# Optimization experiments

Hardware: AMD Instinct MI355X
Metric: run time of the kernel (lower is better)

## Reference

```python
import jax, jax.numpy as jnp
import numpy as np

B, N_OBJS, HW = 2, 30, 64
W_H = HW * HW                      # 4096 visual tokens
N = W_H + 4 * N_OBJS + 64          # 4280 total tokens (satisfies the N - 4*n_objs - 64 == 64*64 check)
QUERY_DIM, HEADS, DIM_HEAD = 320, 8, 40
INNER = HEADS * DIM_HEAD


def setup_inputs() -> dict:
    key = jax.random.key(0)
    ks = jax.random.split(key, 7)
    x = jax.random.normal(ks[0], (B, N, QUERY_DIM), dtype=jnp.float32)
    # binary per-object instance masks on the 64x64 visual grid
    att_masks = (jax.random.uniform(ks[1], (B, N_OBJS, HW, HW)) < 0.15).astype(jnp.float32)
    s = 0.02
    Wq = jax.random.normal(ks[2], (QUERY_DIM, INNER), dtype=jnp.float32) * s
    Wk = jax.random.normal(ks[3], (QUERY_DIM, INNER), dtype=jnp.float32) * s
    Wv = jax.random.normal(ks[4], (QUERY_DIM, INNER), dtype=jnp.float32) * s
    Wo = jax.random.normal(ks[5], (INNER, QUERY_DIM), dtype=jnp.float32) * s
    bo = jax.random.normal(ks[6], (QUERY_DIM,), dtype=jnp.float32) * s
    return {"x": x, "att_masks": att_masks, "Wq": Wq, "Wk": Wk, "Wv": Wv, "Wo": Wo, "bo": bo}


def _build_mask(att_masks):
    # att_masks: [B, n_objs, 64, 64] -> additive/boolean grounding mask [B, 1, N, N]
    b, n_objs = att_masks.shape[0], att_masks.shape[1]
    m = att_masks.reshape(b, n_objs, W_H)                     # [B, O, 4096]
    # sum over objects of per-object outer products (bmm then sum over objs)
    ind = jnp.einsum('boi,boj->bij', m, m)                    # [B, 4096, 4096]
    # visual_token_masks ends up exactly 1 where ind>=1 else 0 (the two masked assigns)
    visual = (ind >= 1.0).astype(att_masks.dtype)
    mask = jnp.ones((b, 1, N, N), dtype=att_masks.dtype)
    mask = mask.at[:, :, :W_H, :W_H].set(visual[:, None])
    mr = m[:, None]                                           # [B, 1, O, 4096]
    rep_rows = jnp.tile(mr, (1, 1, 4, 1))                     # [B, 1, 4O, 4096]
    mask = mask.at[:, :, W_H:N - 64, :W_H].set(rep_rows)
    mask = mask.at[:, :, W_H + n_objs:W_H + 3 * n_objs, :W_H].set(1.0)
    rep_cols = jnp.tile(jnp.swapaxes(mr, 2, 3), (1, 1, 1, 4))  # [B, 1, 4096, 4O]
    mask = mask.at[:, :, :W_H, W_H:N - 64].set(rep_cols)
    mask = mask.at[:, :, :W_H, W_H + n_objs:W_H + 3 * n_objs].set(1.0)
    mask = mask + jnp.eye(N, dtype=att_masks.dtype)[None, None] * 1e-9
    return mask


def reference(x, att_masks, Wq, Wk, Wv, Wo, bo):
    b, n, _ = x.shape
    scale = DIM_HEAD ** -0.5
    q = (x @ Wq).reshape(b, n, HEADS, DIM_HEAD).transpose(0, 2, 1, 3)  # [B,H,N,C]
    k = (x @ Wk).reshape(b, n, HEADS, DIM_HEAD).transpose(0, 2, 1, 3)
    v = (x @ Wv).reshape(b, n, HEADS, DIM_HEAD).transpose(0, 2, 1, 3)
    mask = _build_mask(att_masks)                                      # [B,1,N,N]
    sim = jnp.einsum('bhic,bhjc->bhij', q, k) * scale                  # [B,H,N,N]
    sim = jnp.where(mask <= 0.0, -jnp.inf, sim)
    attn = jax.nn.softmax(sim, axis=-1)
    out = jnp.einsum('bhij,bhjc->bhic', attn, v)                       # [B,H,N,C]
    out = out.transpose(0, 2, 1, 3).reshape(b, n, INNER)
    return out @ Wo + bo
```

## Files before the change

### kernel.cpp

```cpp
#include <hip/hip_runtime.h>
#include <hip/hip_bf16.h>

#define BB 2
#define N_TOK 4280
#define NPAD 4352
#define MPAD 8576
#define WH 4096
#define NOBJ 30
#define QDIM 320
#define HEADS 8
#define DHEAD 40
#define M_ROWS (BB * N_TOK)
#define NT64 (NPAD / 64)
#define NQT (NPAD / 128)
#define KSPLIT 4
#define NTH (NT64 / KSPLIT)

typedef __attribute__((ext_vector_type(8))) short short8;
typedef __attribute__((ext_vector_type(4))) short short4v;
typedef __attribute__((ext_vector_type(4))) float f32x4;
typedef __attribute__((ext_vector_type(4))) unsigned uintx4;

#define GLD16(lds, g) __builtin_amdgcn_global_load_lds( \
    (const __attribute__((address_space(1))) unsigned*)(g), \
    (__attribute__((address_space(3))) unsigned*)(lds), 16, 0, 0)
#define GLD4(lds, g) __builtin_amdgcn_global_load_lds( \
    (const __attribute__((address_space(1))) unsigned*)(g), \
    (__attribute__((address_space(3))) unsigned*)(lds), 4, 0, 0)

__device__ __forceinline__ ushort f2bf(float x) {
    union { __hip_bfloat16 h; ushort u; } cv;
    cv.h = __float2bfloat16(x);
    return cv.u;
}
__device__ __forceinline__ float bf2f(ushort u) {
    union { unsigned u; float f; } cv;
    cv.u = ((unsigned)u) << 16;
    return cv.f;
}

__global__ void k_pre(const float* __restrict__ x, ushort* __restrict__ xb,
                      const float* __restrict__ att, unsigned* __restrict__ bits,
                      unsigned* __restrict__ MQK) {
    int gid = blockIdx.x * blockDim.x + threadIdx.x;
    if (gid < 32) MQK[gid] = 0;
    if (gid < BB * NPAD) {
        int b = gid / NPAD, i = gid - b * NPAD;
        unsigned v = 0;
        if (i < WH) {
            const float* base = att + (size_t)b * NOBJ * WH + i;
            #pragma unroll
            for (int o = 0; o < NOBJ; ++o)
                if (base[(size_t)o * WH] > 0.5f) v |= (1u << o);
        }
        bits[gid] = v;
    }
    if (gid >= M_ROWS * QDIM / 8) return;
    float4 v0 = ((const float4*)x)[gid * 2];
    float4 v1 = ((const float4*)x)[gid * 2 + 1];
    short8 o;
    o[0] = (short)f2bf(v0.x); o[1] = (short)f2bf(v0.y);
    o[2] = (short)f2bf(v0.z); o[3] = (short)f2bf(v0.w);
    o[4] = (short)f2bf(v1.x); o[5] = (short)f2bf(v1.y);
    o[6] = (short)f2bf(v1.z); o[7] = (short)f2bf(v1.w);
    ((short8*)xb)[gid] = o;
}

__global__ __launch_bounds__(256) void k_wcvt(const float* __restrict__ Wq,
                                              const float* __restrict__ Wk,
                                              const float* __restrict__ Wv,
                                              const float* __restrict__ Wo,
                                              ushort* __restrict__ WtAll) {
    __shared__ float T[32][33];
    const int k0 = blockIdx.x * 32;
    const int np0 = blockIdx.y * 32;
    const float SC = 0.15811388300841897f * 1.4426950408889634f;
    const float* src; int n0; float sc = 1.f;
    if (np0 < 320)      { src = Wq; n0 = np0;       sc = SC; }
    else if (np0 < 640) { src = Wk; n0 = np0 - 320; }
    else if (np0 < 960) { src = Wv; n0 = np0 - 640; }
    else                { src = Wo; n0 = np0 - 960; }
    const int tid = threadIdx.x;
    #pragma unroll
    for (int it = 0; it < 4; ++it) {
        int idx = tid + it * 256;
        int r = idx >> 5, c = idx & 31;
        T[r][c] = src[(size_t)(k0 + r) * QDIM + n0 + c];
    }
    __syncthreads();
    #pragma unroll
    for (int it = 0; it < 4; ++it) {
        int idx = tid + it * 256;
        int rr = idx >> 5, cc = idx & 31;
        WtAll[(size_t)(np0 + rr) * QDIM + k0 + cc] = f2bf(T[cc][rr] * sc);
    }
}

template<int IS_OUT>
__global__ __launch_bounds__(256) void k_mm(const ushort* __restrict__ A,
                                            const ushort* __restrict__ Wt,
                                            const float* __restrict__ bias,
                                            ushort* __restrict__ Qb,
                                            ushort* __restrict__ Kb,
                                            ushort* __restrict__ Vt,
                                            float* __restrict__ Cout) {
    __shared__ __align__(16) char Ab[2][8192];
    __shared__ __align__(16) char Bb[2][8192];
    const int tid = threadIdx.x, lane = tid & 63, wv = tid >> 6;
    const int g = lane >> 4, c16 = lane & 15, l7 = lane & 7;
    const int rsub = lane >> 3, slotx = lane & 7;
    const int m0 = blockIdx.x * 64;
    const int nt = blockIdx.y;

    f32x4 acc[4] = {{0,0,0,0},{0,0,0,0},{0,0,0,0},{0,0,0,0}};

    auto STAGE = [&](int ks, int bufi) {
        const int k0 = ks * 64;
        #pragma unroll
        for (int u = 0; u < 2; ++u) {
            int r0 = wv * 16 + u * 8;
            int row = r0 + rsub;
            int slot = slotx ^ (row & 7);
            GLD16(Ab[bufi] + r0 * 128, A + (size_t)(m0 + row) * QDIM + k0 + slot * 8);
            GLD16(Bb[bufi] + r0 * 128, Wt + (size_t)(nt * 64 + row) * QDIM + k0 + slot * 8);
        }
    };

    const int sl0 = (g ^ l7) * 16, sl1 = ((4 + g) ^ l7) * 16;

    STAGE(0, 0);
    __syncthreads();
    int cur = 0;
    for (int ks = 0; ks < 5; ++ks) {
        if (ks < 4) STAGE(ks + 1, cur ^ 1);
        const char* bbase = Bb[cur] + (wv * 16 + c16) * 128;
        short8 bf0 = *(const short8*)(bbase + sl0);
        short8 bf1 = *(const short8*)(bbase + sl1);
        #pragma unroll
        for (int mi = 0; mi < 4; ++mi) {
            const char* abase = Ab[cur] + (mi * 16 + c16) * 128;
            acc[mi] = __builtin_amdgcn_mfma_f32_16x16x32_bf16(*(const short8*)(abase + sl0), bf0, acc[mi], 0, 0, 0);
            acc[mi] = __builtin_amdgcn_mfma_f32_16x16x32_bf16(*(const short8*)(abase + sl1), bf1, acc[mi], 0, 0, 0);
        }
        __syncthreads();
        cur ^= 1;
    }

    const int ng = nt * 64 + wv * 16 + c16;
    if (IS_OUT) {
        float bv = bias[ng];
        #pragma unroll
        for (int mi = 0; mi < 4; ++mi)
            #pragma unroll
            for (int r = 0; r < 4; ++r) {
                int m = m0 + mi * 16 + g * 4 + r;
                if (m < M_ROWS) Cout[(size_t)m * QDIM + ng] = acc[mi][r] + bv;
            }
    } else {
        int p = ng / QDIM, nn = ng - p * QDIM;
        int h = nn / DHEAD, d = nn - h * DHEAD;
        if (p == 2) {
            #pragma unroll
            for (int mi = 0; mi < 4; ++mi) {
                int m = m0 + mi * 16 + g * 4;
                if (m >= M_ROWS) continue;
                int b = m / N_TOK, tok = m - b * N_TOK;
                short4v w4;
                w4[0] = (short)f2bf(acc[mi][0]);
                w4[1] = (short)f2bf(acc[mi][1]);
                w4[2] = (short)f2bf(acc[mi][2]);
                w4[3] = (short)f2bf(acc[mi][3]);
                *(short4v*)(Vt + ((size_t)(b * HEADS + h) * 48 + d) * NPAD + tok) = w4;
            }
        } else {
            ushort* base = (p == 0) ? Qb : Kb;
            #pragma unroll
            for (int mi = 0; mi < 4; ++mi)
                #pragma unroll
                for (int r = 0; r < 4; ++r) {
                    int m = m0 + mi * 16 + g * 4 + r;
                    if (m >= M_ROWS) continue;
                    int b = m / N_TOK, tok = m - b * N_TOK;
                    base[((size_t)(b * HEADS + h) * NPAD + tok) * 64 + d] = f2bf(acc[mi][r]);
                }
        }
    }
}

__global__ __launch_bounds__(256) void k_norm(const ushort* __restrict__ Qb,
                                              const ushort* __restrict__ Kb,
                                              unsigned* __restrict__ MQK) {
    __shared__ float rq[256], rk[256];
    const int bh = blockIdx.x >> 3, part = blockIdx.x & 7;
    const int tid = threadIdx.x;
    float mq = 0.f, mk = 0.f;
    for (int tok = part * 256 + tid; tok < N_TOK; tok += 2048) {
        const ushort* qp = Qb + ((size_t)bh * NPAD + tok) * 64;
        const ushort* kp = Kb + ((size_t)bh * NPAD + tok) * 64;
        float sq = 0.f, sk = 0.f;
        #pragma unroll
        for (int d8 = 0; d8 < 40; d8 += 8) {
            short8 a = *(const short8*)(qp + d8);
            short8 c = *(const short8*)(kp + d8);
            #pragma unroll
            for (int j = 0; j < 8; ++j) {
                float fa = bf2f((ushort)a[j]), fc = bf2f((ushort)c[j]);
                sq += fa * fa; sk += fc * fc;
            }
        }
        mq = fmaxf(mq, sq); mk = fmaxf(mk, sk);
    }
    rq[tid] = mq; rk[tid] = mk;
    __syncthreads();
    for (int s = 128; s > 0; s >>= 1) {
        if (tid < s) {
            rq[tid] = fmaxf(rq[tid], rq[tid + s]);
            rk[tid] = fmaxf(rk[tid], rk[tid + s]);
        }
        __syncthreads();
    }
    if (tid == 0) {
        atomicMax(&MQK[bh],      __float_as_uint(rq[0]));
        atomicMax(&MQK[16 + bh], __float_as_uint(rk[0]));
    }
}

__global__ void k_patch(ushort* __restrict__ Qb, ushort* __restrict__ Kb,
                        ushort* __restrict__ Vt, const unsigned* __restrict__ MQK) {
    int gid = blockIdx.x * blockDim.x + threadIdx.x;
    if (gid >= 16 * NPAD) return;
    int bh = gid / NPAD, tok = gid - bh * NPAD;
    float B = sqrtf(__uint_as_float(MQK[bh])) * sqrtf(__uint_as_float(MQK[16 + bh]));
    Qb[(size_t)gid * 64 + 40] = f2bf(-B);
    short8 z = {0, 0, 0, 0, 0, 0, 0, 0};
    short8 k1 = z;
    k1[0] = (short)((tok < N_TOK) ? 0x3F80 : 0);
    ushort* krow = Kb + (size_t)gid * 64;
    *(short8*)(krow + 40) = k1;
    *(short8*)(krow + 48) = z;
    *(short8*)(krow + 56) = z;
    Vt[((size_t)bh * 48 + 40) * NPAD + tok] = (tok < N_TOK) ? (ushort)0x3F80 : (ushort)0;
}

__device__ __forceinline__ bool mask_ok(int i, int j, unsigned bi, unsigned bj) {
    if (j >= N_TOK) return false;
    if (i == j) return true;
    if (i < WH) {
        if (j < WH) return (bi & bj) != 0u;
        if (j >= WH + 4 * NOBJ) return true;
        int cI = j - WH;
        if ((unsigned)(cI - NOBJ) < (unsigned)(2 * NOBJ)) return true;
        int om = (cI < NOBJ) ? cI : cI - 3 * NOBJ;
        return ((bi >> om) & 1u) != 0u;
    }
    if (j >= WH) return true;
    if (i >= WH + 4 * NOBJ) return true;
    int rI = i - WH;
    if ((unsigned)(rI - NOBJ) < (unsigned)(2 * NOBJ)) return true;
    int om = (rI < NOBJ) ? rI : rI - 3 * NOBJ;
    return ((bj >> om) & 1u) != 0u;
}

__global__ __launch_bounds__(256, 4) void k_attn(const ushort* __restrict__ Qb,
                                                 const ushort* __restrict__ Kb,
                                                 const ushort* __restrict__ Vt,
                                                 const unsigned* __restrict__ bits,
                                                 ushort* __restrict__ Opart,
                                                 float* __restrict__ Lpart) {
    __shared__ __align__(16) char KtB[64 * 128];
    __shared__ __align__(16) char VtB[48 * 128];
    __shared__ __align__(16) char PsB[4 * 4096];
    __shared__ __align__(16) unsigned bJB[64];

    const int tid = threadIdx.x;
    const int lane = tid & 63, wv = tid >> 6;
    const int g = lane >> 4, c16 = lane & 15;
    const int l7x = c16 & 7;
    const int rsub = lane >> 3, slotx = lane & 7;

    const int bid = blockIdx.x;
    const int logical = (bid & 7) * 272 + (bid >> 3);
    const int grp = logical / NQT;
    const int qt = logical - grp * NQT;
    const int bh = grp >> 2, ks = grp & 3;
    const int b = bh >> 3;
    const int q0w = qt * 128 + wv * 32;
    const int iqA = q0w + c16, iqB = iqA + 16;
    const bool vis_i = (qt < 32);
    const int t0 = ks * NTH;

    short8 qA0, qA1, qB0, qB1;
    {
        const ushort* qp = Qb + ((size_t)bh * NPAD + iqA) * 64 + g * 8;
        qA0 = *(const short8*)(qp);
        qA1 = *(const short8*)(qp + 32);
        qB0 = *(const short8*)(qp + 16 * 64);
        qB1 = *(const short8*)(qp + 16 * 64 + 32);
    }
    const unsigned bI_A = bits[(size_t)b * NPAD + iqA];
    const unsigned bI_B = bits[(size_t)b * NPAD + iqB];

    const ushort* kp = Kb + ((size_t)bh * NPAD + t0 * 64 + wv * 16 + rsub) * 64 + (slotx ^ rsub) * 8;
    const ushort* vbase = Vt + (size_t)bh * 48 * NPAD;
    int voff0 = 0, voff1 = 0;
    if (wv < 3) {
        int d0 = wv * 16 + rsub, d1 = d0 + 8;
        voff0 = d0 * NPAD + (slotx ^ rsub) * 8;
        voff1 = d1 * NPAD + (slotx ^ rsub) * 8;
    }
    const unsigned* bp = bits + (size_t)b * NPAD + t0 * 64 + lane;

    auto STAGE_K = [&](const ushort* kpt) {
        GLD16(KtB + (wv * 16) * 128, kpt);
        GLD16(KtB + (wv * 16 + 8) * 128, kpt + 512);
    };
    auto STAGE_V = [&](int j0) {
        if (wv < 3) {
            GLD16(VtB + (wv * 16) * 128, vbase + j0 + voff0);
            GLD16(VtB + (wv * 16 + 8) * 128, vbase + j0 + voff1);
        }
    };
    auto STAGE_B = [&](const unsigned* bpt) {
        if (wv == 3) GLD4(bJB, bpt);
    };

    const int sl0 = (g ^ l7x) * 16;
    const int sl1 = ((4 + g) ^ l7x) * 16;
    const int pswA = wv * 4096 + c16 * 128;
    const int pswB = pswA + 2048;
    const int swz = l7x << 4;

    f32x4 oA0 = {0,0,0,0}, oA1 = oA0, oA2 = oA0;
    f32x4 oB0 = oA0, oB1 = oA0, oB2 = oA0;

    STAGE_K(kp); STAGE_V(t0 * 64); STAGE_B(bp);
    __syncthreads();

    for (int t = 0; t < NTH; ++t) {
        const int tg = t0 + t;
        const int j0 = tg * 64;

        auto do_tile = [&](auto okA_fn, auto okB_fn) {
            #pragma unroll
            for (int kt = 0; kt < 4; ++kt) {
                const char* arow = KtB + (kt * 16 + c16) * 128;
                short8 a0 = *(const short8*)(arow + sl0);
                short8 a1 = *(const short8*)(arow + sl1);
                f32x4 sA = {0,0,0,0}, sB = {0,0,0,0};
                __builtin_amdgcn_s_setprio(1);
                sA = __builtin_amdgcn_mfma_f32_16x16x32_bf16(a0, qA0, sA, 0, 0, 0);
                sA = __builtin_amdgcn_mfma_f32_16x16x32_bf16(a1, qA1, sA, 0, 0, 0);
                sB = __builtin_amdgcn_mfma_f32_16x16x32_bf16(a0, qB0, sB, 0, 0, 0);
                sB = __builtin_amdgcn_mfma_f32_16x16x32_bf16(a1, qB1, sB, 0, 0, 0);
                __builtin_amdgcn_s_setprio(0);
                uintx4 bk = *(const uintx4*)&bJB[kt * 16 + g * 4];
                float pA[4], pB[4];
                #pragma unroll
                for (int r = 0; r < 4; ++r) {
                    int j = j0 + kt * 16 + g * 4 + r;
                    float eA = __builtin_amdgcn_exp2f(sA[r]);
                    float eB = __builtin_amdgcn_exp2f(sB[r]);
                    pA[r] = okA_fn(j, bk[r]) ? eA : 0.f;
                    pB[r] = okB_fn(j, bk[r]) ? eB : 0.f;
                }
                unsigned wA0, wA1, wB0, wB1;
                asm("v_cvt_pk_bf16_f32 %0, %1, %2" : "=v"(wA0) : "v"(pA[0]), "v"(pA[1]));
                asm("v_cvt_pk_bf16_f32 %0, %1, %2" : "=v"(wA1) : "v"(pA[2]), "v"(pA[3]));
                asm("v_cvt_pk_bf16_f32 %0, %1, %2" : "=v"(wB0) : "v"(pB[0]), "v"(pB[1]));
                asm("v_cvt_pk_bf16_f32 %0, %1, %2" : "=v"(wB1) : "v"(pB[2]), "v"(pB[3]));
                uint2 vA; vA.x = wA0; vA.y = wA1;
                uint2 vB; vB.x = wB0; vB.y = wB1;
                int po = (kt * 32 + g * 8) ^ swz;
                *(uint2*)(PsB + pswA + po) = vA;
                *(uint2*)(PsB + pswB + po) = vB;
            }
        };

        const bool vis_j = (j0 + 64 <= WH);
        if (vis_i && vis_j && ((tg >> 1) != qt)) {
            do_tile([&](int j, unsigned bj) { return (bI_A & bj) != 0u; },
                    [&](int j, unsigned bj) { return (bI_B & bj) != 0u; });
        } else if (vis_i && vis_j) {
            do_tile([&](int j, unsigned bj) { return ((bI_A & bj) != 0u) || (iqA == j); },
                    [&](int j, unsigned bj) { return ((bI_B & bj) != 0u) || (iqB == j); });
        } else {
            do_tile([&](int j, unsigned bj) { return mask_ok(iqA, j, bI_A, bj); },
                    [&](int j, unsigned bj) { return mask_ok(iqB, j, bI_B, bj); });
        }

        __syncthreads();
        kp += 64 * 64; bp += 64;
        if (t + 1 < NTH) { STAGE_K(kp); STAGE_B(bp); }

        short8 paA0 = *(const short8*)(PsB + pswA + sl0);
        short8 paA1 = *(const short8*)(PsB + pswA + sl1);
        short8 paB0 = *(const short8*)(PsB + pswB + sl0);
        short8 paB1 = *(const short8*)(PsB + pswB + sl1);
        {
            const char* v0r = VtB + (0 * 16 + c16) * 128;
            const char* v1r = VtB + (1 * 16 + c16) * 128;
            const char* v2r = VtB + (2 * 16 + c16) * 128;
            short8 v00 = *(const short8*)(v0r + sl0), v01 = *(const short8*)(v0r + sl1);
            short8 v10 = *(const short8*)(v1r + sl0), v11 = *(const short8*)(v1r + sl1);
            short8 v20 = *(const short8*)(v2r + sl0), v21 = *(const short8*)(v2r + sl1);
            __builtin_amdgcn_s_setprio(1);
            oA0 = __builtin_amdgcn_mfma_f32_16x16x32_bf16(paA0, v00, oA0, 0, 0, 0);
            oA0 = __builtin_amdgcn_mfma_f32_16x16x32_bf16(paA1, v01, oA0, 0, 0, 0);
            oB0 = __builtin_amdgcn_mfma_f32_16x16x32_bf16(paB0, v00, oB0, 0, 0, 0);
            oB0 = __builtin_amdgcn_mfma_f32_16x16x32_bf16(paB1, v01, oB0, 0, 0, 0);
            oA1 = __builtin_amdgcn_mfma_f32_16x16x32_bf16(paA0, v10, oA1, 0, 0, 0);
            oA1 = __builtin_amdgcn_mfma_f32_16x16x32_bf16(paA1, v11, oA1, 0, 0, 0);
            oB1 = __builtin_amdgcn_mfma_f32_16x16x32_bf16(paB0, v10, oB1, 0, 0, 0);
            oB1 = __builtin_amdgcn_mfma_f32_16x16x32_bf16(paB1, v11, oB1, 0, 0, 0);
            oA2 = __builtin_amdgcn_mfma_f32_16x16x32_bf16(paA0, v20, oA2, 0, 0, 0);
            oA2 = __builtin_amdgcn_mfma_f32_16x16x32_bf16(paA1, v21, oA2, 0, 0, 0);
            oB2 = __builtin_amdgcn_mfma_f32_16x16x32_bf16(paB0, v20, oB2, 0, 0, 0);
            oB2 = __builtin_amdgcn_mfma_f32_16x16x32_bf16(paB1, v21, oB2, 0, 0, 0);
            __builtin_amdgcn_s_setprio(0);
        }

        __syncthreads();
        if (t + 1 < NTH) STAGE_V((tg + 1) * 64);
    }

    const size_t prow = ((size_t)ks * 16 + bh) * NPAD;
    if (c16 == 8) {
        #pragma unroll
        for (int r = 0; r < 4; ++r) {
            Lpart[prow + q0w + g * 4 + r]      = oA2[r];
            Lpart[prow + q0w + 16 + g * 4 + r] = oB2[r];
        }
    }
    #pragma unroll
    for (int r = 0; r < 4; ++r) {
        int qrA = q0w + g * 4 + r;
        int qrB = qrA + 16;
        if (qrA < N_TOK) {
            ushort* dst = Opart + (prow + qrA) * 40;
            dst[c16]      = f2bf(oA0[r]);
            dst[16 + c16] = f2bf(oA1[r]);
            if (c16 < 8) dst[32 + c16] = f2bf(oA2[r]);
        }
        if (qrB < N_TOK) {
            ushort* dst = Opart + (prow + qrB) * 40;
            dst[c16]      = f2bf(oB0[r]);
            dst[16 + c16] = f2bf(oB1[r]);
            if (c16 < 8) dst[32 + c16] = f2bf(oB2[r]);
        }
    }
}

__global__ __launch_bounds__(256) void k_comb(const ushort* __restrict__ Opart,
                                              const float* __restrict__ Lpart,
                                              ushort* __restrict__ AOb) {
    int gid = blockIdx.x * blockDim.x + threadIdx.x;
    if (gid >= 16 * N_TOK * 10) return;
    int row = gid / 10, v = gid - row * 10;
    int bh = row / N_TOK, q = row - bh * N_TOK;
    f32x4 s = {0.f, 0.f, 0.f, 0.f};
    float l = 0.f;
    #pragma unroll
    for (int ks = 0; ks < KSPLIT; ++ks) {
        size_t rr = ((size_t)ks * 16 + bh) * NPAD + q;
        short4v a = *(const short4v*)(Opart + rr * 40 + v * 4);
        s[0] += bf2f((ushort)a[0]); s[1] += bf2f((ushort)a[1]);
        s[2] += bf2f((ushort)a[2]); s[3] += bf2f((ushort)a[3]);
        l += Lpart[rr];
    }
    float inv = 1.f / l;
    int b = bh >> 3, h = bh & 7;
    short4v o;
    o[0] = (short)f2bf(s[0] * inv);
    o[1] = (short)f2bf(s[1] * inv);
    o[2] = (short)f2bf(s[2] * inv);
    o[3] = (short)f2bf(s[3] * inv);
    *(short4v*)(AOb + (size_t)(b * N_TOK + q) * QDIM + h * DHEAD + v * 4) = o;
}

extern "C" void kernel_launch(void* const* d_in, const int* in_sizes, int n_in,
                              void* d_out, int out_size, void* d_ws, size_t ws_size,
                              hipStream_t stream) {
    const float* x   = (const float*)d_in[0];
    const float* att = (const float*)d_in[1];
    const float* Wq  = (const float*)d_in[2];
    const float* Wk  = (const float*)d_in[3];
    const float* Wv  = (const float*)d_in[4];
    const float* Wo  = (const float*)d_in[5];
    const float* bo  = (const float*)d_in[6];
    float* out = (float*)d_out;

    char* w = (char*)d_ws;
    unsigned* bits = (unsigned*)w;
    unsigned* MQK = (unsigned*)(w + 40960);
    size_t off = 65536;
    ushort* xb    = (ushort*)(w + off); off += (size_t)MPAD * QDIM * 2;
    ushort* WtAll = (ushort*)(w + off); off += (size_t)1280 * QDIM * 2;
    ushort* Qb    = (ushort*)(w + off); off += (size_t)16 * NPAD * 64 * 2;
    ushort* Kb    = (ushort*)(w + off); off += (size_t)16 * NPAD * 64 * 2;
    ushort* Vt    = (ushort*)(w + off); off += (size_t)16 * 48 * NPAD * 2;
    ushort* AOb   = (ushort*)(w + off); off += (size_t)MPAD * QDIM * 2;
    ushort* Opart = (ushort*)(w + off); off += (size_t)KSPLIT * 16 * NPAD * 40 * 2;
    float*  Lpart = (float*)(w + off);

    k_pre<<<(M_ROWS * QDIM / 8 + 255) / 256, 256, 0, stream>>>(x, xb, att, bits, MQK);
    k_wcvt<<<dim3(10, 40), 256, 0, stream>>>(Wq, Wk, Wv, Wo, WtAll);

    k_mm<0><<<dim3(MPAD / 64, 15), 256, 0, stream>>>(xb, WtAll, nullptr, Qb, Kb, Vt, nullptr);
    k_norm<<<128, 256, 0, stream>>>(Qb, Kb, MQK);
    k_patch<<<(16 * NPAD + 255) / 256, 256, 0, stream>>>(Qb, Kb, Vt, MQK);
    k_attn<<<16 * NQT * KSPLIT, 256, 0, stream>>>(Qb, Kb, Vt, bits, Opart, Lpart);
    k_comb<<<(16 * N_TOK * 10 + 255) / 256, 256, 0, stream>>>(Opart, Lpart, AOb);
    k_mm<1><<<dim3(MPAD / 64, 5), 256, 0, stream>>>(AOb, WtAll + 960 * QDIM, bo,
                                                    nullptr, nullptr, nullptr, out);
}
```

Before: 179.8 us.

## Double-buffer K and mask bits in LDS and read V straight into registers

```diff
diff --git a/kernel.cpp b/kernel.cpp
--- a/kernel.cpp
+++ b/kernel.cpp
@@ -267,10 +267,9 @@
                                                  const unsigned* __restrict__ bits,
                                                  ushort* __restrict__ Opart,
                                                  float* __restrict__ Lpart) {
-    __shared__ __align__(16) char KtB[64 * 128];
-    __shared__ __align__(16) char VtB[48 * 128];
+    __shared__ __align__(16) char KtB[2][8192];
     __shared__ __align__(16) char PsB[4 * 4096];
-    __shared__ __align__(16) unsigned bJB[64];
+    __shared__ __align__(16) unsigned bJB[2][64];
 
     const int tid = threadIdx.x;
     const int lane = tid & 63, wv = tid >> 6;
@@ -301,27 +300,17 @@
     const unsigned bI_B = bits[(size_t)b * NPAD + iqB];
 
     const ushort* kp = Kb + ((size_t)bh * NPAD + t0 * 64 + wv * 16 + rsub) * 64 + (slotx ^ rsub) * 8;
-    const ushort* vbase = Vt + (size_t)bh * 48 * NPAD;
-    int voff0 = 0, voff1 = 0;
-    if (wv < 3) {
-        int d0 = wv * 16 + rsub, d1 = d0 + 8;
-        voff0 = d0 * NPAD + (slotx ^ rsub) * 8;
-        voff1 = d1 * NPAD + (slotx ^ rsub) * 8;
-    }
     const unsigned* bp = bits + (size_t)b * NPAD + t0 * 64 + lane;
-
-    auto STAGE_K = [&](const ushort* kpt) {
-        GLD16(KtB + (wv * 16) * 128, kpt);
-        GLD16(KtB + (wv * 16 + 8) * 128, kpt + 512);
+    const ushort* v0p = Vt + ((size_t)bh * 48 +  0 + c16) * NPAD + t0 * 64 + g * 8;
+    const ushort* v1p = v0p + (size_t)16 * NPAD;
+    const ushort* v2p = v1p + (size_t)16 * NPAD;
+
+    auto STAGE_K = [&](const ushort* kpt, int bi) {
+        GLD16(KtB[bi] + (wv * 16) * 128, kpt);
+        GLD16(KtB[bi] + (wv * 16 + 8) * 128, kpt + 512);
     };
-    auto STAGE_V = [&](int j0) {
-        if (wv < 3) {
-            GLD16(VtB + (wv * 16) * 128, vbase + j0 + voff0);
-            GLD16(VtB + (wv * 16 + 8) * 128, vbase + j0 + voff1);
-        }
-    };
-    auto STAGE_B = [&](const unsigned* bpt) {
-        if (wv == 3) GLD4(bJB, bpt);
+    auto STAGE_B = [&](const unsigned* bpt, int bi) {
+        if (wv == 3) GLD4(bJB[bi], bpt);
     };
 
     const int sl0 = (g ^ l7x) * 16;
@@ -333,17 +322,25 @@
     f32x4 oA0 = {0,0,0,0}, oA1 = oA0, oA2 = oA0;
     f32x4 oB0 = oA0, oB1 = oA0, oB2 = oA0;
 
-    STAGE_K(kp); STAGE_V(t0 * 64); STAGE_B(bp);
+    STAGE_K(kp, 0); STAGE_B(bp, 0);
     __syncthreads();
+    int cur = 0;
 
     for (int t = 0; t < NTH; ++t) {
         const int tg = t0 + t;
         const int j0 = tg * 64;
 
+        short8 v00 = *(const short8*)(v0p), v01 = *(const short8*)(v0p + 32);
+        short8 v10 = *(const short8*)(v1p), v11 = *(const short8*)(v1p + 32);
+        short8 v20 = *(const short8*)(v2p), v21 = *(const short8*)(v2p + 32);
+
+        kp += 64 * 64; bp += 64;
+        if (t + 1 < NTH) { STAGE_K(kp, cur ^ 1); STAGE_B(bp, cur ^ 1); }
+
         auto do_tile = [&](auto okA_fn, auto okB_fn) {
             #pragma unroll
             for (int kt = 0; kt < 4; ++kt) {
-                const char* arow = KtB + (kt * 16 + c16) * 128;
+                const char* arow = KtB[cur] + (kt * 16 + c16) * 128;
                 short8 a0 = *(const short8*)(arow + sl0);
                 short8 a1 = *(const short8*)(arow + sl1);
                 f32x4 sA = {0,0,0,0}, sB = {0,0,0,0};
@@ -353,7 +350,7 @@
                 sB = __builtin_amdgcn_mfma_f32_16x16x32_bf16(a0, qB0, sB, 0, 0, 0);
                 sB = __builtin_amdgcn_mfma_f32_16x16x32_bf16(a1, qB1, sB, 0, 0, 0);
                 __builtin_amdgcn_s_setprio(0);
-                uintx4 bk = *(const uintx4*)&bJB[kt * 16 + g * 4];
+                uintx4 bk = *(const uintx4*)&bJB[cur][kt * 16 + g * 4];
                 float pA[4], pB[4];
                 #pragma unroll
                 for (int r = 0; r < 4; ++r) {
@@ -388,21 +385,11 @@
                     [&](int j, unsigned bj) { return mask_ok(iqB, j, bI_B, bj); });
         }
 
-        __syncthreads();
-        kp += 64 * 64; bp += 64;
-        if (t + 1 < NTH) { STAGE_K(kp); STAGE_B(bp); }
-
         short8 paA0 = *(const short8*)(PsB + pswA + sl0);
         short8 paA1 = *(const short8*)(PsB + pswA + sl1);
         short8 paB0 = *(const short8*)(PsB + pswB + sl0);
         short8 paB1 = *(const short8*)(PsB + pswB + sl1);
         {
-            const char* v0r = VtB + (0 * 16 + c16) * 128;
-            const char* v1r = VtB + (1 * 16 + c16) * 128;
-            const char* v2r = VtB + (2 * 16 + c16) * 128;
-            short8 v00 = *(const short8*)(v0r + sl0), v01 = *(const short8*)(v0r + sl1);
-            short8 v10 = *(const short8*)(v1r + sl0), v11 = *(const short8*)(v1r + sl1);
-            short8 v20 = *(const short8*)(v2r + sl0), v21 = *(const short8*)(v2r + sl1);
             __builtin_amdgcn_s_setprio(1);
             oA0 = __builtin_amdgcn_mfma_f32_16x16x32_bf16(paA0, v00, oA0, 0, 0, 0);
             oA0 = __builtin_amdgcn_mfma_f32_16x16x32_bf16(paA1, v01, oA0, 0, 0, 0);
@@ -419,8 +406,9 @@
             __builtin_amdgcn_s_setprio(0);
         }
 
+        v0p += 64; v1p += 64; v2p += 64;
         __syncthreads();
-        if (t + 1 < NTH) STAGE_V((tg + 1) * 64);
+        cur ^= 1;
     }
 
     const size_t prow = ((size_t)ks * 16 + bh) * NPAD;
```

Result: slower. 217.3 us (+20.9%).
